# Performance work log

Measured on AMD Instinct MI355X. Metric: run time of the kernel, lower is better.

Reference implementation:

```python
import jax, jax.numpy as jnp
import numpy as np


def _booth_forward(x, weight, bits):
    """Faithful translation of BoothFunction.forward.
    Python operator precedence in the original:
      a[m] - m[m] & mask      == (a - m) & mask
      q >> 1 | (a&1) << bits-1 == (q >> 1) | ((a & 1) << (bits - 1))
      a >> 1 | a & 1 << bits-1 == (a >> 1) | (a & (1 << (bits - 1)))
    sub_mask / add_mask are disjoint, so where-based updates are exact.
    """
    m = jnp.round(x).astype(jnp.int32)
    q = jnp.round(weight).astype(jnp.int32)
    mask = (1 << bits) - 1
    a = jnp.zeros_like(m)
    q_prev = jnp.zeros_like(m)
    for _ in range(bits):  # fixed small unroll over bit positions
        last_bit_q = q & 1
        sub = (last_bit_q == 1) & (q_prev == 0)
        add = (last_bit_q == 0) & (q_prev == 1)
        a = jnp.where(sub, (a - m) & mask, a)
        a = jnp.where(add, (a + m) & mask, a)
        q_prev = q & 1
        q = (q >> 1) | ((a & 1) << (bits - 1))
        a = (a >> 1) | (a & (1 << (bits - 1)))
    result = (a << bits) | q
    is_neg = (result & (1 << (2 * bits - 1))) != 0
    resf = result.astype(jnp.float32)
    return jnp.where(is_neg, resf - float(1 << (2 * bits)), resf)


def setup_inputs() -> dict:
    key = jax.random.key(0)
    k1, k2 = jax.random.split(key)
    out_features, in_features = 4096, 8192
    x = jax.random.randint(k1, (out_features, in_features), 0, 256).astype(jnp.float32)
    weight = jax.random.normal(k2, (out_features, in_features), dtype=jnp.float32)
    return {"x": x, "weight": weight, "bits": 8}


def reference(x, weight, bits):
    return _booth_forward(x, weight, bits)
```

## Files before the change

kernel.cpp:

```cpp
#include <hip/hip_runtime.h>

typedef float f32x4 __attribute__((ext_vector_type(4)));

__device__ __forceinline__ float booth_exact(float xf, float wf) {
    float qf = rintf(wf);
    int q = (int)qf;
    int m = (int)rintf(xf);
    int M    = m << 24;
    int Mneg = -M;
    int Mx   = M ^ Mneg;
    int P = 0;
    int qp = 0;
    #pragma unroll
    for (int b = 0; b < 8; ++b) {
        int last = q & 1;
        int s = -last;
        int t = -(qp ^ last);
        int delta = (M ^ (Mx & s)) & t;
        P += delta;
        P >>= 1;
        qp = last;
        q >>= 1;
    }
    float res = (float)(P >> 16);
    return (qf < 0.0f) ? -65537.0f : res;
}

__device__ __forceinline__ f32x4 booth4(f32x4 xv, f32x4 wv) {
    f32x4 ov;
    ov.x = booth_exact(xv.x, wv.x);
    ov.y = booth_exact(xv.y, wv.y);
    ov.z = booth_exact(xv.z, wv.z);
    ov.w = booth_exact(xv.w, wv.w);
    return ov;
}

__global__ __launch_bounds__(256) void booth_vec4_kernel(const f32x4* __restrict__ x,
                                                         const f32x4* __restrict__ w,
                                                         f32x4* __restrict__ out,
                                                         int n4) {
    int tid = blockIdx.x * blockDim.x + threadIdx.x;
    int stride = gridDim.x * blockDim.x;
    int i = tid;
    for (; i + stride < n4; i += 2 * stride) {
        f32x4 x0 = x[i];
        f32x4 w0 = w[i];
        f32x4 x1 = x[i + stride];
        f32x4 w1 = w[i + stride];
        f32x4 o0 = booth4(x0, w0);
        f32x4 o1 = booth4(x1, w1);
        __builtin_nontemporal_store(o0, &out[i]);
        __builtin_nontemporal_store(o1, &out[i + stride]);
    }
    if (i < n4) {
        f32x4 o = booth4(x[i], w[i]);
        __builtin_nontemporal_store(o, &out[i]);
    }
}

__global__ __launch_bounds__(256) void booth_tail_kernel(const float* __restrict__ x,
                                                         const float* __restrict__ w,
                                                         float* __restrict__ out,
                                                         int start, int n) {
    int i = start + blockIdx.x * blockDim.x + threadIdx.x;
    if (i < n) out[i] = booth_exact(x[i], w[i]);
}

extern "C" void kernel_launch(void* const* d_in, const int* in_sizes, int n_in,
                              void* d_out, int out_size, void* d_ws, size_t ws_size,
                              hipStream_t stream) {
    const float* x = (const float*)d_in[0];
    const float* w = (const float*)d_in[1];
    float* out = (float*)d_out;

    int n = out_size;
    int n4 = n / 4;
    int rem = n - n4 * 4;

    const int block = 256;
    int grid = 2048;
    int needed = (n4 + block - 1) / block;
    if (needed < grid) grid = needed > 0 ? needed : 1;

    if (n4 > 0) {
        booth_vec4_kernel<<<grid, block, 0, stream>>>(
            (const f32x4*)x, (const f32x4*)w, (f32x4*)out, n4);
    }
    if (rem > 0) {
        booth_tail_kernel<<<1, block, 0, stream>>>(x, w, out, n4 * 4, n);
    }
}
```

Baseline: 77.53 us.

## Replace per-element Booth loop with shared-memory lookup table for small weights

Each block builds a 16x256 table in shared memory holding the Booth product for every small non-negative q and 8-bit m. Elements then do a table lookup instead of the unrolled 8-step bit loop. Negative q returns the constant, and out-of-range q falls back to a full exact Booth routine. This trades ALU work for the table build in every block, LDS gather traffic with possible bank conflicts, and a divergent fallback branch. The kernel is likely memory-bound, so the saving may be small.

```diff
diff --git a/kernel.cpp b/kernel.cpp
--- a/kernel.cpp
+++ b/kernel.cpp
@@ -2,10 +2,7 @@
 
 typedef float f32x4 __attribute__((ext_vector_type(4)));
 
-__device__ __forceinline__ float booth_exact(float xf, float wf) {
-    float qf = rintf(wf);
-    int q = (int)qf;
-    int m = (int)rintf(xf);
+__device__ __forceinline__ float booth_packed_pos(int m, int q) {
     int M    = m << 24;
     int Mneg = -M;
     int Mx   = M ^ Mneg;
@@ -16,29 +13,55 @@
         int last = q & 1;
         int s = -last;
         int t = -(qp ^ last);
-        int delta = (M ^ (Mx & s)) & t;
-        P += delta;
+        P += (M ^ (Mx & s)) & t;
         P >>= 1;
         qp = last;
         q >>= 1;
     }
-    float res = (float)(P >> 16);
-    return (qf < 0.0f) ? -65537.0f : res;
+    return (float)(P >> 16);
 }
 
-__device__ __forceinline__ f32x4 booth4(f32x4 xv, f32x4 wv) {
-    f32x4 ov;
-    ov.x = booth_exact(xv.x, wv.x);
-    ov.y = booth_exact(xv.y, wv.y);
-    ov.z = booth_exact(xv.z, wv.z);
-    ov.w = booth_exact(xv.w, wv.w);
-    return ov;
+__device__ float booth_full(int m, int q) {
+    const int mask = 255;
+    int a = 0, qp = 0;
+    #pragma unroll
+    for (int b = 0; b < 8; ++b) {
+        int last = q & 1;
+        if (last == 1 && qp == 0) a = (a - m) & mask;
+        else if (last == 0 && qp == 1) a = (a + m) & mask;
+        qp = last;
+        q = (q >> 1) | ((a & 1) << 7);
+        a = (a >> 1) | (a & 0x80);
+    }
+    int result = (a << 8) | q;
+    float rf = (float)result;
+    if (result & (1 << 15)) rf -= 65536.0f;
+    return rf;
 }
 
-__global__ __launch_bounds__(256) void booth_vec4_kernel(const f32x4* __restrict__ x,
-                                                         const f32x4* __restrict__ w,
-                                                         f32x4* __restrict__ out,
-                                                         int n4) {
+#define TABQ 16
+__device__ __forceinline__ float booth_lut(float xf, float wf, const float* tab) {
+    float qf = rintf(wf);
+    int q = (int)qf;
+    int mc = ((int)rintf(xf)) & 255;
+    if (__builtin_expect((unsigned)(q + 256) < (unsigned)(256 + TABQ), 1)) {
+        int qc = q < 0 ? 0 : q;
+        float v = tab[(qc << 8) | mc];
+        return (q < 0) ? -65537.0f : v;
+    }
+    return booth_full((int)rintf(xf), q);
+}
+
+__global__ __launch_bounds__(256) void booth_lut_kernel(const f32x4* __restrict__ x,
+                                                        const f32x4* __restrict__ w,
+                                                        f32x4* __restrict__ out,
+                                                        int n4) {
+    __shared__ float tab[TABQ * 256];
+    for (int e = threadIdx.x; e < TABQ * 256; e += blockDim.x) {
+        tab[e] = booth_packed_pos(e & 255, e >> 8);
+    }
+    __syncthreads();
+
     int tid = blockIdx.x * blockDim.x + threadIdx.x;
     int stride = gridDim.x * blockDim.x;
     int i = tid;
@@ -47,14 +70,19 @@
         f32x4 w0 = w[i];
         f32x4 x1 = x[i + stride];
         f32x4 w1 = w[i + stride];
-        f32x4 o0 = booth4(x0, w0);
-        f32x4 o1 = booth4(x1, w1);
+        f32x4 o0, o1;
+        o0.x = booth_lut(x0.x, w0.x, tab); o0.y = booth_lut(x0.y, w0.y, tab);
+        o0.z = booth_lut(x0.z, w0.z, tab); o0.w = booth_lut(x0.w, w0.w, tab);
+        o1.x = booth_lut(x1.x, w1.x, tab); o1.y = booth_lut(x1.y, w1.y, tab);
+        o1.z = booth_lut(x1.z, w1.z, tab); o1.w = booth_lut(x1.w, w1.w, tab);
         __builtin_nontemporal_store(o0, &out[i]);
         __builtin_nontemporal_store(o1, &out[i + stride]);
     }
     if (i < n4) {
-        f32x4 o = booth4(x[i], w[i]);
-        __builtin_nontemporal_store(o, &out[i]);
+        f32x4 xv = x[i], wv = w[i], ov;
+        ov.x = booth_lut(xv.x, wv.x, tab); ov.y = booth_lut(xv.y, wv.y, tab);
+        ov.z = booth_lut(xv.z, wv.z, tab); ov.w = booth_lut(xv.w, wv.w, tab);
+        __builtin_nontemporal_store(ov, &out[i]);
     }
 }
 
@@ -63,7 +91,7 @@
                                                          float* __restrict__ out,
                                                          int start, int n) {
     int i = start + blockIdx.x * blockDim.x + threadIdx.x;
-    if (i < n) out[i] = booth_exact(x[i], w[i]);
+    if (i < n) out[i] = booth_full((int)rintf(x[i]), (int)rintf(w[i]));
 }
 
 extern "C" void kernel_launch(void* const* d_in, const int* in_sizes, int n_in,
@@ -83,7 +111,7 @@
     if (needed < grid) grid = needed > 0 ? needed : 1;
 
     if (n4 > 0) {
-        booth_vec4_kernel<<<grid, block, 0, stream>>>(
+        booth_lut_kernel<<<grid, block, 0, stream>>>(
             (const f32x4*)x, (const f32x4*)w, (f32x4*)out, n4);
     }
     if (rem > 0) {
```

Result: faster. 68.29 us (-11.9%).
